# Kernel optimization log

Measured on AMD Instinct MI355X. Metric: run time of the kernel, lower is better.

Reference implementation:

```python
import jax, jax.numpy as jnp
import numpy as np

B, D, S = 16384, 2048, 512      # batch, input_dim, sideinfo_dim
E, H1, H2 = 8, 1024, 512        # subexpert_num, subexpert_unit
EPS = 1e-5                       # BatchNorm eps (torch default)


def setup_inputs() -> dict:
    key = jax.random.key(0)
    ks = jax.random.split(key, 16)
    inp = {
        "input": jax.random.normal(ks[0], (B, D), jnp.float32),
        "sideinfo": jax.random.normal(ks[1], (B, S), jnp.float32),
        # expert layer 1: Linear(D->H1) per expert, batched over E
        "W1": jax.random.normal(ks[2], (E, D, H1), jnp.float32) / np.sqrt(D),
        "b1": jax.random.normal(ks[3], (E, H1), jnp.float32) * 0.01,
        "gamma1": 1.0 + 0.01 * jax.random.normal(ks[4], (E, H1), jnp.float32),
        "beta1": jax.random.normal(ks[5], (E, H1), jnp.float32) * 0.01,
        "mean1": jax.random.normal(ks[6], (E, H1), jnp.float32) * 0.01,
        "var1": jax.random.uniform(ks[7], (E, H1), jnp.float32, 0.5, 1.5),
        # expert layer 2: Linear(H1->H2) per expert
        "W2": jax.random.normal(ks[8], (E, H1, H2), jnp.float32) / np.sqrt(H1),
        "b2": jax.random.normal(ks[9], (E, H2), jnp.float32) * 0.01,
        "gamma2": 1.0 + 0.01 * jax.random.normal(ks[10], (E, H2), jnp.float32),
        "beta2": jax.random.normal(ks[11], (E, H2), jnp.float32) * 0.01,
        "mean2": jax.random.normal(ks[12], (E, H2), jnp.float32) * 0.01,
        "var2": jax.random.uniform(ks[13], (E, H2), jnp.float32, 0.5, 1.5),
        # gate: Linear(S->E) + softmax
        "Wg": jax.random.normal(ks[14], (S, E), jnp.float32) / np.sqrt(S),
        "bg": jax.random.normal(ks[15], (E,), jnp.float32) * 0.01,
    }
    return inp


def _bn(x, gamma, beta, mean, var):
    # eval-mode BatchNorm1d with per-expert running stats; x: [B,E,H]
    return (x - mean) * (gamma * jax.lax.rsqrt(var + EPS)) + beta


def reference(input, sideinfo, W1, b1, gamma1, beta1, mean1, var1,
              W2, b2, gamma2, beta2, mean2, var2, Wg, bg):
    # all E expert MLPs as two batched GEMMs (dropout is identity in eval)
    h = jnp.einsum('bd,edh->beh', input, W1) + b1            # [B,E,H1]
    h = jax.nn.relu(_bn(h, gamma1, beta1, mean1, var1))
    o = jnp.einsum('beh,eho->beo', h, W2) + b2               # [B,E,H2]
    o = jax.nn.relu(_bn(o, gamma2, beta2, mean2, var2))
    gate = jax.nn.softmax(sideinfo @ Wg + bg, axis=1)        # [B,E]
    return jnp.einsum('beo,be->bo', o, gate)                 # [B,H2]
```

## Files before the change

### kernel.cpp

```cpp
#include <hip/hip_runtime.h>
#include <hip/hip_bf16.h>

static constexpr int B_  = 16384;
static constexpr int D_  = 2048;
static constexpr int S_  = 512;
static constexpr int E_  = 8;
static constexpr int H1_ = 1024;
static constexpr int H2_ = 512;
static constexpr float EPS_ = 1e-5f;

typedef __bf16 bf16x8 __attribute__((ext_vector_type(8)));
typedef float  f32x4  __attribute__((ext_vector_type(4)));

static __device__ __forceinline__ unsigned short f2bf(float f) {
    unsigned u = __float_as_uint(f);
    unsigned r = (u + 0x7fffu + ((u >> 16) & 1u)) >> 16;
    return (unsigned short)r;
}


__global__ void cvt_bf16_kernel(const float* __restrict__ in, ushort* __restrict__ out, long n) {
    long i = ((long)blockIdx.x * blockDim.x + threadIdx.x) * 4;
    long stride = (long)gridDim.x * blockDim.x * 4;
    for (; i < n; i += stride) {
        float4 v = *(const float4*)(in + i);
        ushort4 o;
        o.x = f2bf(v.x); o.y = f2bf(v.y); o.z = f2bf(v.z); o.w = f2bf(v.w);
        *(ushort4*)(out + i) = o;
    }
}

__global__ void transpose_cvt_kernel(const float* __restrict__ in, ushort* __restrict__ out,
                                     int R, int C) {
    __shared__ float t[64][65];
    int nbr = R >> 6, nbc = C >> 6;
    int bid = blockIdx.x;
    int e = bid / (nbr * nbc);
    int rem = bid % (nbr * nbc);
    int br = (rem / nbc) << 6, bc = (rem % nbc) << 6;
    const float* ip = in + (size_t)e * R * C;
    ushort* op = out + (size_t)e * R * C;
    int tcol = (threadIdx.x & 15) * 4;
    int trow = threadIdx.x >> 4;
#pragma unroll
    for (int p = 0; p < 4; p++) {
        int r = trow + p * 16;
        float4 v = *(const float4*)(ip + (size_t)(br + r) * C + bc + tcol);
        t[r][tcol + 0] = v.x; t[r][tcol + 1] = v.y; t[r][tcol + 2] = v.z; t[r][tcol + 3] = v.w;
    }
    __syncthreads();
#pragma unroll
    for (int p = 0; p < 4; p++) {
        int c = trow + p * 16;
        ushort4 o;
        o.x = f2bf(t[tcol + 0][c]);
        o.y = f2bf(t[tcol + 1][c]);
        o.z = f2bf(t[tcol + 2][c]);
        o.w = f2bf(t[tcol + 3][c]);
        *(ushort4*)(op + (size_t)(bc + c) * R + br + tcol) = o;
    }
}

__global__ void fold_bn_kernel(const float* __restrict__ gamma, const float* __restrict__ beta,
                               const float* __restrict__ mean, const float* __restrict__ var,
                               const float* __restrict__ bias,
                               float* __restrict__ Sv, float* __restrict__ Tv, int n) {
    int i = blockIdx.x * 256 + threadIdx.x;
    if (i < n) {
        float s = gamma[i] * rsqrtf(var[i] + EPS_);
        Sv[i] = s;
        Tv[i] = (bias[i] - mean[i]) * s + beta[i];
    }
}

__global__ void gate_kernel(const float* __restrict__ side, const float* __restrict__ Wg,
                            const float* __restrict__ bg, float* __restrict__ gate) {
    int wid = threadIdx.x >> 6, lane = threadIdx.x & 63;
    int b = blockIdx.x * 4 + wid;
    const float* sp = side + (size_t)b * S_ + lane * 8;
    float4 v0 = *(const float4*)sp;
    float4 v1 = *(const float4*)(sp + 4);
    float sv[8] = {v0.x, v0.y, v0.z, v0.w, v1.x, v1.y, v1.z, v1.w};
    float acc[E_] = {0,0,0,0,0,0,0,0};
    const float* wrow = Wg + (size_t)(lane * 8) * E_;
#pragma unroll
    for (int j = 0; j < 8; j++) {
        float4 w0 = *(const float4*)(wrow + j * E_);
        float4 w1 = *(const float4*)(wrow + j * E_ + 4);
        acc[0] += sv[j] * w0.x; acc[1] += sv[j] * w0.y;
        acc[2] += sv[j] * w0.z; acc[3] += sv[j] * w0.w;
        acc[4] += sv[j] * w1.x; acc[5] += sv[j] * w1.y;
        acc[6] += sv[j] * w1.z; acc[7] += sv[j] * w1.w;
    }
#pragma unroll
    for (int off = 32; off; off >>= 1)
#pragma unroll
        for (int e = 0; e < E_; e++) acc[e] += __shfl_xor(acc[e], off, 64);
    float m = -1e30f;
#pragma unroll
    for (int e = 0; e < E_; e++) { acc[e] += bg[e]; m = fmaxf(m, acc[e]); }
    float s = 0.f;
#pragma unroll
    for (int e = 0; e < E_; e++) { acc[e] = __expf(acc[e] - m); s += acc[e]; }
    float inv = 1.f / s;
    if (lane < E_) gate[(size_t)b * E_ + lane] = acc[lane] * inv;
}


__device__ __forceinline__ void g2lds16(const void* g, void* l) {
    __builtin_amdgcn_global_load_lds((const __attribute__((address_space(1))) unsigned int*)g,
                                     (__attribute__((address_space(3))) unsigned int*)l,
                                     16, 0, 0);
}

#define BAR()      asm volatile("s_barrier" ::: "memory")
#define WAITVM(n)  asm volatile("s_waitcnt vmcnt(" #n ")" ::: "memory")
#define MFMA(a,b,c) __builtin_amdgcn_mfma_f32_16x16x32_bf16((a),(b),(c),0,0,0)


template<int EPI>
__global__ __launch_bounds__(1024, 4)
void gemm8(const ushort* __restrict__ A, const ushort* __restrict__ Bt, long aBatch,
           const float* __restrict__ Sv, const float* __restrict__ Tv,
           ushort* __restrict__ hout, float* __restrict__ outp, const float* __restrict__ gate,
           int M, int N, int K, int tilesN, int tilesM)
{
    extern __shared__ char smem[];

    const int NT  = K >> 6;
    const int tpe = tilesM * tilesN;

    const int nwg = gridDim.x, per = nwg >> 3;
    const int b0  = blockIdx.x;
    const int bid = (b0 & 7) * per + (b0 >> 3);

    const int e   = bid / tpe;
    const int rem = bid % tpe;
    const int tm  = rem / tilesN, tn = rem % tilesN;

    const char* aBase = (const char*)(A + (size_t)e * aBatch + (size_t)tm * 256 * K);
    const char* bBase = (const char*)(Bt + (size_t)e * N * K + (size_t)tn * 256 * K);
    const size_t rowB = (size_t)K * 2;
    const size_t half1 = 128 * rowB;

    const int tid = threadIdx.x, w = tid >> 6, lane = tid & 63;
    const int wm = w >> 2, wn = w & 3;

    const int srow = tid >> 3;
    const int scol_sw = ((tid & 7) * 16) ^ ((srow & 7) << 4);
    const int ldsW = w * 1024;

    const int lr = lane & 15;
    const int cks0 = ((lane >> 4) * 16) ^ ((lane & 7) << 4);
    const int cks1 = (64 + (lane >> 4) * 16) ^ ((lane & 7) << 4);
    const char* rdA0 = smem + 98304 + (wm * 64 + lr) * 128 + cks0;
    const char* rdA1 = smem + 98304 + (wm * 64 + lr) * 128 + cks1;
    const char* rdB0 = smem + (wn * 64 + lr) * 128 + cks0;
    const char* rdB1 = smem + (wn * 64 + lr) * 128 + cks1;

#define STG2T(gp, ldsoff) do { \
        g2lds16((gp), smem + (ldsoff) + ldsW); \
        g2lds16((gp) + half1, smem + (ldsoff) + 16384 + ldsW); } while (0)

    const char* ga = aBase + (size_t)srow * rowB + scol_sw;
    const char* gb = bBase + (size_t)srow * rowB + scol_sw;

    f32x4 acc[4][4] = {};
    bf16x8 a[4], b[4];

    int bCur = 0, bN1 = 32768, bN2 = 65536;

    STG2T(ga,       98304);
    STG2T(gb,       0);
    STG2T(gb + 128, 32768);
    WAITVM(2);
    BAR();

    const char* spA = ga + 128;
    const char* spB = gb + 256;

    for (int t = 0; t < NT; ++t) {
        const int bi    = t & 1;
        const int oRA   = bi * 32768;
        const int oSA   = 98304 + (bi ^ 1) * 32768;
        const bool moreA = (t < NT - 1);
        const bool moreB = (t < NT - 2);

#pragma unroll
        for (int mf = 0; mf < 4; ++mf) a[mf] = *(const bf16x8*)(rdA0 + oRA + mf * 2048);
#pragma unroll
        for (int nf = 0; nf < 4; ++nf) b[nf] = *(const bf16x8*)(rdB0 + bCur + nf * 2048);
        if (moreA) STG2T(spA, oSA);
        __builtin_amdgcn_s_setprio(1);
#pragma unroll
        for (int mf = 0; mf < 4; ++mf)
#pragma unroll
            for (int nf = 0; nf < 4; ++nf)
                acc[mf][nf] = MFMA(a[mf], b[nf], acc[mf][nf]);
        __builtin_amdgcn_s_setprio(0);

#pragma unroll
        for (int mf = 0; mf < 4; ++mf) a[mf] = *(const bf16x8*)(rdA1 + oRA + mf * 2048);
#pragma unroll
        for (int nf = 0; nf < 4; ++nf) b[nf] = *(const bf16x8*)(rdB1 + bCur + nf * 2048);
        if (moreB) STG2T(spB, bN2);
        __builtin_amdgcn_s_setprio(1);
#pragma unroll
        for (int mf = 0; mf < 4; ++mf)
#pragma unroll
            for (int nf = 0; nf < 4; ++nf)
                acc[mf][nf] = MFMA(a[mf], b[nf], acc[mf][nf]);
        __builtin_amdgcn_s_setprio(0);

        if (moreA) {
            if (moreB) { WAITVM(2); } else { WAITVM(0); }
            BAR();
        }

        spA += 128; spB += 128;
        const int tb = bCur; bCur = bN1; bN1 = bN2; bN2 = tb;
    }

    const int rbase = tm * 256 + wm * 64 + (lane >> 4) * 4;
    const int cbase = tn * 256 + wn * 64 + lr;
    if (EPI == 1) {
#pragma unroll
        for (int nf = 0; nf < 4; ++nf) {
            const int col = cbase + nf * 16;
            const float s = Sv[e * N + col];
            const float tt = Tv[e * N + col];
#pragma unroll
            for (int mf = 0; mf < 4; ++mf) {
                const int row0 = rbase + mf * 16;
                f32x4 v = acc[mf][nf];
#pragma unroll
                for (int r = 0; r < 4; ++r) {
                    float x = v[r] * s + tt;
                    x = x > 0.f ? x : 0.f;
                    hout[((size_t)e * M + row0 + r) * N + col] = f2bf(x);
                }
            }
        }
    }
#undef STG2T
}


__global__ __launch_bounds__(512, 2)
void gemm2e(const ushort* __restrict__ H, const ushort* __restrict__ W2T,
            const float* __restrict__ Sv, const float* __restrict__ Tv,
            const float* __restrict__ gate, float* __restrict__ outp)
{
    extern __shared__ char smem[];

    const int b0 = blockIdx.x;
    const int bid = (b0 & 7) * 32 + (b0 >> 3);
    const int tm = bid >> 1, tn = bid & 1;

    const size_t rowB  = (size_t)H1_ * 2;
    const size_t strAE = (size_t)B_ * H1_ * 2;
    const size_t strBE = (size_t)H2_ * H1_ * 2;
    const size_t half2 = 64 * rowB;
    const size_t halfB = 128 * rowB;

    const int tid = threadIdx.x, w = tid >> 6, lane = tid & 63;
    const int wm = w >> 2, wn = w & 3;

    const int srow = tid >> 3;
    const int scol_sw = ((tid & 7) * 16) ^ ((srow & 7) << 4);
    const int ldsW = w * 1024;

    const int lr = lane & 15;
    const int cks0 = ((lane >> 4) * 16) ^ ((lane & 7) << 4);
    const int cks1 = (64 + (lane >> 4) * 16) ^ ((lane & 7) << 4);
    const char* rdA0 = smem + (wm * 64 + lr) * 128 + cks0;
    const char* rdA1 = smem + (wm * 64 + lr) * 128 + cks1;
    const char* rdB0 = smem + (wn * 64 + lr) * 128 + cks0;
    const char* rdB1 = smem + (wn * 64 + lr) * 128 + cks1;

    const char* ga = (const char*)H + (size_t)tm * 128 * rowB + (size_t)srow * rowB + scol_sw;
    const char* gb = (const char*)W2T + (size_t)tn * 256 * rowB + (size_t)srow * rowB + scol_sw;

#define STG6(gAp, gBp, aOff, bOff) do { \
        g2lds16((gAp),                 smem + (aOff) + 0     + ldsW); \
        g2lds16((gAp) + half2,         smem + (aOff) + 8192  + ldsW); \
        g2lds16((gBp),                 smem + (bOff) + 0     + ldsW); \
        g2lds16((gBp) + half2,         smem + (bOff) + 8192  + ldsW); \
        g2lds16((gBp) + halfB,         smem + (bOff) + 16384 + ldsW); \
        g2lds16((gBp) + halfB + half2, smem + (bOff) + 24576 + ldsW); } while (0)

    f32x4 acc[4][4] = {};
    f32x4 oacc[4][4] = {};
    bf16x8 a0[4], a1[4], b0v[4], b1v[4];

    int aCur = 98304, aN1 = 114688, aN2 = 131072;
    int bCur = 0,     bN1 = 32768,  bN2 = 65536;

    STG6(ga, gb, aCur, bCur);
    STG6(ga + 128, gb + 128, aN1, bN1);
    WAITVM(6);
    BAR();

#pragma unroll
    for (int mf = 0; mf < 4; ++mf) a0[mf] = *(const bf16x8*)(rdA0 + aCur + mf * 2048);
#pragma unroll
    for (int nf = 0; nf < 4; ++nf) b0v[nf] = *(const bf16x8*)(rdB0 + bCur + nf * 2048);

    const int rbase = tm * 128 + wm * 64 + (lane >> 4) * 4;
    const int cbase = tn * 256 + wn * 64 + lr;

    for (int t = 0; t < 128; ++t) {
        const int t2 = t + 2;
        const bool moreS = (t2 < 128);
        const bool moreT = (t < 127);

        const char* gA2 = ga + (size_t)(t2 >> 4) * strAE + (t2 & 15) * 128;
        const char* gB2 = gb + (size_t)(t2 >> 4) * strBE + (t2 & 15) * 128;

#pragma unroll
        for (int mf = 0; mf < 4; ++mf) a1[mf] = *(const bf16x8*)(rdA1 + aCur + mf * 2048);
#pragma unroll
        for (int nf = 0; nf < 4; ++nf) b1v[nf] = *(const bf16x8*)(rdB1 + bCur + nf * 2048);
        if (moreS) STG6(gA2, gB2, aN2, bN2);
        __builtin_amdgcn_s_setprio(1);
#pragma unroll
        for (int mf = 0; mf < 4; ++mf)
#pragma unroll
            for (int nf = 0; nf < 4; ++nf)
                acc[mf][nf] = MFMA(a0[mf], b0v[nf], acc[mf][nf]);
        __builtin_amdgcn_s_setprio(0);

        __builtin_amdgcn_s_setprio(1);
#pragma unroll
        for (int mf = 0; mf < 4; ++mf)
#pragma unroll
            for (int nf = 0; nf < 4; ++nf)
                acc[mf][nf] = MFMA(a1[mf], b1v[nf], acc[mf][nf]);
        __builtin_amdgcn_s_setprio(0);

        if (moreT) {
            if (moreS) { WAITVM(6); } else { WAITVM(0); }
            BAR();
#pragma unroll
            for (int mf = 0; mf < 4; ++mf) a0[mf] = *(const bf16x8*)(rdA0 + aN1 + mf * 2048);
#pragma unroll
            for (int nf = 0; nf < 4; ++nf) b0v[nf] = *(const bf16x8*)(rdB0 + bN1 + nf * 2048);
        }

        if ((t & 15) == 15) {
            const int e = t >> 4;
            float sc[4], tc[4];
#pragma unroll
            for (int nf = 0; nf < 4; ++nf) {
                sc[nf] = Sv[e * H2_ + cbase + nf * 16];
                tc[nf] = Tv[e * H2_ + cbase + nf * 16];
            }
#pragma unroll
            for (int mf = 0; mf < 4; ++mf) {
#pragma unroll
                for (int r = 0; r < 4; ++r) {
                    const int row = rbase + mf * 16 + r;
                    const float g = gate[(size_t)row * E_ + e];
#pragma unroll
                    for (int nf = 0; nf < 4; ++nf) {
                        float x = acc[mf][nf][r] * sc[nf] + tc[nf];
                        x = x > 0.f ? x : 0.f;
                        oacc[mf][nf][r] += g * x;
                    }
                }
            }
#pragma unroll
            for (int mf = 0; mf < 4; ++mf)
#pragma unroll
                for (int nf = 0; nf < 4; ++nf)
                    acc[mf][nf] = (f32x4){0.f, 0.f, 0.f, 0.f};
        }

        const int ta = aCur; aCur = aN1; aN1 = aN2; aN2 = ta;
        const int tb = bCur; bCur = bN1; bN1 = bN2; bN2 = tb;
    }

#pragma unroll
    for (int mf = 0; mf < 4; ++mf) {
#pragma unroll
        for (int r = 0; r < 4; ++r) {
            const int row = rbase + mf * 16 + r;
#pragma unroll
            for (int nf = 0; nf < 4; ++nf)
                outp[(size_t)row * H2_ + cbase + nf * 16] = oacc[mf][nf][r];
        }
    }
#undef STG6
}


extern "C" void kernel_launch(void* const* d_in, const int* in_sizes, int n_in,
                              void* d_out, int out_size, void* d_ws, size_t ws_size,
                              hipStream_t stream) {
    (void)in_sizes; (void)n_in; (void)out_size; (void)ws_size;

    const float* input    = (const float*)d_in[0];
    const float* sideinfo = (const float*)d_in[1];
    const float* W1   = (const float*)d_in[2];
    const float* b1   = (const float*)d_in[3];
    const float* g1   = (const float*)d_in[4];
    const float* be1  = (const float*)d_in[5];
    const float* m1   = (const float*)d_in[6];
    const float* v1   = (const float*)d_in[7];
    const float* W2   = (const float*)d_in[8];
    const float* b2   = (const float*)d_in[9];
    const float* g2   = (const float*)d_in[10];
    const float* be2  = (const float*)d_in[11];
    const float* m2   = (const float*)d_in[12];
    const float* v2   = (const float*)d_in[13];
    const float* Wg   = (const float*)d_in[14];
    const float* bg   = (const float*)d_in[15];

    char* w = (char*)d_ws;
    size_t off = 0;
    auto carve = [&](size_t bytes) {
        void* p = w + off;
        off += (bytes + 255) & ~(size_t)255;
        return p;
    };
    ushort* Abf  = (ushort*)carve((size_t)B_ * D_ * 2);
    ushort* W1T  = (ushort*)carve((size_t)E_ * H1_ * D_ * 2);
    ushort* W2T  = (ushort*)carve((size_t)E_ * H2_ * H1_ * 2);
    ushort* hbuf = (ushort*)carve((size_t)E_ * B_ * H1_ * 2);
    float*  S1   = (float*)carve((size_t)E_ * H1_ * 4);
    float*  T1   = (float*)carve((size_t)E_ * H1_ * 4);
    float*  S2   = (float*)carve((size_t)E_ * H2_ * 4);
    float*  T2   = (float*)carve((size_t)E_ * H2_ * 4);
    float*  gatep = (float*)carve((size_t)B_ * E_ * 4);

    float* outp = (float*)d_out;

    hipFuncSetAttribute(reinterpret_cast<const void*>(&gemm8<1>),
                        hipFuncAttributeMaxDynamicSharedMemorySize, 163840);
    hipFuncSetAttribute(reinterpret_cast<const void*>(&gemm2e),
                        hipFuncAttributeMaxDynamicSharedMemorySize, 147456);

    cvt_bf16_kernel<<<4096, 256, 0, stream>>>(input, Abf, (long)B_ * D_);
    transpose_cvt_kernel<<<E_ * (D_ / 64) * (H1_ / 64), 256, 0, stream>>>(W1, W1T, D_, H1_);
    transpose_cvt_kernel<<<E_ * (H1_ / 64) * (H2_ / 64), 256, 0, stream>>>(W2, W2T, H1_, H2_);
    fold_bn_kernel<<<(E_ * H1_ + 255) / 256, 256, 0, stream>>>(g1, be1, m1, v1, b1, S1, T1, E_ * H1_);
    fold_bn_kernel<<<(E_ * H2_ + 255) / 256, 256, 0, stream>>>(g2, be2, m2, v2, b2, S2, T2, E_ * H2_);
    gate_kernel<<<B_ / 4, 256, 0, stream>>>(sideinfo, Wg, bg, gatep);

    gemm8<1><<<E_ * (B_ / 256) * (H1_ / 256), 1024, 163840, stream>>>(
        Abf, W1T, 0L, S1, T1, hbuf, nullptr, nullptr, B_, H1_, D_, H1_ / 256, B_ / 256);

    gemm2e<<<(B_ / 128) * (H2_ / 256), 512, 147456, stream>>>(
        hbuf, W2T, S2, T2, gatep, outp);
}
```

Baseline: 695.9 us.

## Double gemm2e waves to 16 with 32-row warp tiles and fewer registers

The second expert GEMM now runs with 1024 threads (16 waves) per block instead of 512. Each wave covers a 32x64 output tile instead of 64x64, and the staging macro issues three 16-byte global-to-LDS loads per thread instead of six. The register prefetch of the next k-step's fragments across the barrier is removed; both k-halves are now read from LDS inside the iteration. This halves per-wave accumulator and fragment registers to raise wave count and latency hiding, at the cost of losing the cross-barrier LDS prefetch and adding LDS read traffic per MFMA.

```diff
diff --git a/kernel.cpp b/kernel.cpp
--- a/kernel.cpp
+++ b/kernel.cpp
@@ -246,7 +246,7 @@
 }
 
 
-__global__ __launch_bounds__(512, 2)
+__global__ __launch_bounds__(1024, 4)
 void gemm2e(const ushort* __restrict__ H, const ushort* __restrict__ W2T,
             const float* __restrict__ Sv, const float* __restrict__ Tv,
             const float* __restrict__ gate, float* __restrict__ outp)
@@ -260,7 +260,6 @@
     const size_t rowB  = (size_t)H1_ * 2;
     const size_t strAE = (size_t)B_ * H1_ * 2;
     const size_t strBE = (size_t)H2_ * H1_ * 2;
-    const size_t half2 = 64 * rowB;
     const size_t halfB = 128 * rowB;
 
     const int tid = threadIdx.x, w = tid >> 6, lane = tid & 63;
@@ -273,40 +272,32 @@
     const int lr = lane & 15;
     const int cks0 = ((lane >> 4) * 16) ^ ((lane & 7) << 4);
     const int cks1 = (64 + (lane >> 4) * 16) ^ ((lane & 7) << 4);
-    const char* rdA0 = smem + (wm * 64 + lr) * 128 + cks0;
-    const char* rdA1 = smem + (wm * 64 + lr) * 128 + cks1;
+    const char* rdA0 = smem + 98304 + (wm * 32 + lr) * 128 + cks0;
+    const char* rdA1 = smem + 98304 + (wm * 32 + lr) * 128 + cks1;
     const char* rdB0 = smem + (wn * 64 + lr) * 128 + cks0;
     const char* rdB1 = smem + (wn * 64 + lr) * 128 + cks1;
 
     const char* ga = (const char*)H + (size_t)tm * 128 * rowB + (size_t)srow * rowB + scol_sw;
     const char* gb = (const char*)W2T + (size_t)tn * 256 * rowB + (size_t)srow * rowB + scol_sw;
 
-#define STG6(gAp, gBp, aOff, bOff) do { \
-        g2lds16((gAp),                 smem + (aOff) + 0     + ldsW); \
-        g2lds16((gAp) + half2,         smem + (aOff) + 8192  + ldsW); \
-        g2lds16((gBp),                 smem + (bOff) + 0     + ldsW); \
-        g2lds16((gBp) + half2,         smem + (bOff) + 8192  + ldsW); \
-        g2lds16((gBp) + halfB,         smem + (bOff) + 16384 + ldsW); \
-        g2lds16((gBp) + halfB + half2, smem + (bOff) + 24576 + ldsW); } while (0)
-
-    f32x4 acc[4][4] = {};
-    f32x4 oacc[4][4] = {};
-    bf16x8 a0[4], a1[4], b0v[4], b1v[4];
-
-    int aCur = 98304, aN1 = 114688, aN2 = 131072;
-    int bCur = 0,     bN1 = 32768,  bN2 = 65536;
-
-    STG6(ga, gb, aCur, bCur);
-    STG6(ga + 128, gb + 128, aN1, bN1);
-    WAITVM(6);
+#define STG3(gAp, gBp, aOff, bOff) do { \
+        g2lds16((gAp),         smem + (aOff) + ldsW); \
+        g2lds16((gBp),         smem + (bOff) + ldsW); \
+        g2lds16((gBp) + halfB, smem + (bOff) + 16384 + ldsW); } while (0)
+
+    f32x4 acc[2][4] = {};
+    f32x4 oacc[2][4] = {};
+    bf16x8 a[2], b[4];
+
+    int aCurR = 0,     aN1R = 16384, aN2R = 32768;
+    int bCur  = 0,     bN1  = 32768, bN2  = 65536;
+
+    STG3(ga, gb, 98304 + aCurR, bCur);
+    STG3(ga + 128, gb + 128, 98304 + aN1R, bN1);
+    WAITVM(3);
     BAR();
 
-#pragma unroll
-    for (int mf = 0; mf < 4; ++mf) a0[mf] = *(const bf16x8*)(rdA0 + aCur + mf * 2048);
-#pragma unroll
-    for (int nf = 0; nf < 4; ++nf) b0v[nf] = *(const bf16x8*)(rdB0 + bCur + nf * 2048);
-
-    const int rbase = tm * 128 + wm * 64 + (lane >> 4) * 4;
+    const int rbase = tm * 128 + wm * 32 + (lane >> 4) * 4;
     const int cbase = tn * 256 + wn * 64 + lr;
 
     for (int t = 0; t < 128; ++t) {
@@ -318,33 +309,33 @@
         const char* gB2 = gb + (size_t)(t2 >> 4) * strBE + (t2 & 15) * 128;
 
 #pragma unroll
-        for (int mf = 0; mf < 4; ++mf) a1[mf] = *(const bf16x8*)(rdA1 + aCur + mf * 2048);
-#pragma unroll
-        for (int nf = 0; nf < 4; ++nf) b1v[nf] = *(const bf16x8*)(rdB1 + bCur + nf * 2048);
-        if (moreS) STG6(gA2, gB2, aN2, bN2);
+        for (int mf = 0; mf < 2; ++mf) a[mf] = *(const bf16x8*)(rdA0 + aCurR + mf * 2048);
+#pragma unroll
+        for (int nf = 0; nf < 4; ++nf) b[nf] = *(const bf16x8*)(rdB0 + bCur + nf * 2048);
+        if (moreS) STG3(gA2, gB2, 98304 + aN2R, bN2);
         __builtin_amdgcn_s_setprio(1);
 #pragma unroll
-        for (int mf = 0; mf < 4; ++mf)
+        for (int mf = 0; mf < 2; ++mf)
 #pragma unroll
             for (int nf = 0; nf < 4; ++nf)
-                acc[mf][nf] = MFMA(a0[mf], b0v[nf], acc[mf][nf]);
+                acc[mf][nf] = MFMA(a[mf], b[nf], acc[mf][nf]);
         __builtin_amdgcn_s_setprio(0);
 
+#pragma unroll
+        for (int mf = 0; mf < 2; ++mf) a[mf] = *(const bf16x8*)(rdA1 + aCurR + mf * 2048);
+#pragma unroll
+        for (int nf = 0; nf < 4; ++nf) b[nf] = *(const bf16x8*)(rdB1 + bCur + nf * 2048);
         __builtin_amdgcn_s_setprio(1);
 #pragma unroll
-        for (int mf = 0; mf < 4; ++mf)
+        for (int mf = 0; mf < 2; ++mf)
 #pragma unroll
             for (int nf = 0; nf < 4; ++nf)
-                acc[mf][nf] = MFMA(a1[mf], b1v[nf], acc[mf][nf]);
+                acc[mf][nf] = MFMA(a[mf], b[nf], acc[mf][nf]);
         __builtin_amdgcn_s_setprio(0);
 
         if (moreT) {
-            if (moreS) { WAITVM(6); } else { WAITVM(0); }
+            if (moreS) { WAITVM(3); } else { WAITVM(0); }
             BAR();
-#pragma unroll
-            for (int mf = 0; mf < 4; ++mf) a0[mf] = *(const bf16x8*)(rdA0 + aN1 + mf * 2048);
-#pragma unroll
-            for (int nf = 0; nf < 4; ++nf) b0v[nf] = *(const bf16x8*)(rdB0 + bN1 + nf * 2048);
         }
 
         if ((t & 15) == 15) {
@@ -356,7 +347,7 @@
                 tc[nf] = Tv[e * H2_ + cbase + nf * 16];
             }
 #pragma unroll
-            for (int mf = 0; mf < 4; ++mf) {
+            for (int mf = 0; mf < 2; ++mf) {
 #pragma unroll
                 for (int r = 0; r < 4; ++r) {
                     const int row = rbase + mf * 16 + r;
@@ -370,18 +361,18 @@
                 }
             }
 #pragma unroll
-            for (int mf = 0; mf < 4; ++mf)
+            for (int mf = 0; mf < 2; ++mf)
 #pragma unroll
                 for (int nf = 0; nf < 4; ++nf)
                     acc[mf][nf] = (f32x4){0.f, 0.f, 0.f, 0.f};
         }
 
-        const int ta = aCur; aCur = aN1; aN1 = aN2; aN2 = ta;
-        const int tb = bCur; bCur = bN1; bN1 = bN2; bN2 = tb;
-    }
-
-#pragma unroll
-    for (int mf = 0; mf < 4; ++mf) {
+        const int ta = aCurR; aCurR = aN1R; aN1R = aN2R; aN2R = ta;
+        const int tb = bCur;  bCur  = bN1;  bN1  = bN2;  bN2  = tb;
+    }
+
+#pragma unroll
+    for (int mf = 0; mf < 2; ++mf) {
 #pragma unroll
         for (int r = 0; r < 4; ++r) {
             const int row = rbase + mf * 16 + r;
@@ -390,7 +381,7 @@
                 outp[(size_t)row * H2_ + cbase + nf * 16] = oacc[mf][nf][r];
         }
     }
-#undef STG6
+#undef STG3
 }
 
 
@@ -450,6 +441,6 @@
     gemm8<1><<<E_ * (B_ / 256) * (H1_ / 256), 1024, 163840, stream>>>(
         Abf, W1T, 0L, S1, T1, hbuf, nullptr, nullptr, B_, H1_, D_, H1_ / 256, B_ / 256);
 
-    gemm2e<<<(B_ / 128) * (H2_ / 256), 512, 147456, stream>>>(
+    gemm2e<<<(B_ / 128) * (H2_ / 256), 1024, 147456, stream>>>(
         hbuf, W2T, S2, T2, gatep, outp);
 }
```

Result: no change. 704.6 us (+1.2%).

## Shrink first-layer GEMM tile to 256x128 with K=32 triple-buffered stages

Applied to the files above, without the earlier changes.

Retiles the first expert GEMM from 256x256 output tiles with 1024 threads to 256x128 tiles with 512 threads. The K step drops from 64 to 32, and both A and B now use a three-stage LDS ring. The LDS swizzle is redone for 64-byte rows. Dynamic LDS per block falls from 160KB to 72KB, so two blocks may fit per CU, trading fewer, larger tiles for more, smaller ones. The cost is halved reuse of each A tile, which doubles A reloads from global memory, and twice as many barriers per K.

```diff
diff --git a/kernel.cpp b/kernel.cpp
--- a/kernel.cpp
+++ b/kernel.cpp
@@ -119,7 +119,7 @@
 
 
 template<int EPI>
-__global__ __launch_bounds__(1024, 4)
+__global__ __launch_bounds__(512, 4)
 void gemm8(const ushort* __restrict__ A, const ushort* __restrict__ Bt, long aBatch,
            const float* __restrict__ Sv, const float* __restrict__ Tv,
            ushort* __restrict__ hout, float* __restrict__ outp, const float* __restrict__ gate,
@@ -127,7 +127,7 @@
 {
     extern __shared__ char smem[];
 
-    const int NT  = K >> 6;
+    const int NT  = K >> 5;
     const int tpe = tilesM * tilesN;
 
     const int nwg = gridDim.x, per = nwg >> 3;
@@ -139,28 +139,26 @@
     const int tm  = rem / tilesN, tn = rem % tilesN;
 
     const char* aBase = (const char*)(A + (size_t)e * aBatch + (size_t)tm * 256 * K);
-    const char* bBase = (const char*)(Bt + (size_t)e * N * K + (size_t)tn * 256 * K);
+    const char* bBase = (const char*)(Bt + (size_t)e * N * K + (size_t)tn * 128 * K);
     const size_t rowB = (size_t)K * 2;
-    const size_t half1 = 128 * rowB;
+    const size_t halfA = 128 * rowB;
 
     const int tid = threadIdx.x, w = tid >> 6, lane = tid & 63;
-    const int wm = w >> 2, wn = w & 3;
-
-    const int srow = tid >> 3;
-    const int scol_sw = ((tid & 7) * 16) ^ ((srow & 7) << 4);
+    const int wm = w >> 1, wn = w & 1;
+
+    const int srow = tid >> 2;
+    const int scol_sw = (((tid & 3) ^ ((tid >> 3) & 3)) << 4);
     const int ldsW = w * 1024;
 
     const int lr = lane & 15;
-    const int cks0 = ((lane >> 4) * 16) ^ ((lane & 7) << 4);
-    const int cks1 = (64 + (lane >> 4) * 16) ^ ((lane & 7) << 4);
-    const char* rdA0 = smem + 98304 + (wm * 64 + lr) * 128 + cks0;
-    const char* rdA1 = smem + 98304 + (wm * 64 + lr) * 128 + cks1;
-    const char* rdB0 = smem + (wn * 64 + lr) * 128 + cks0;
-    const char* rdB1 = smem + (wn * 64 + lr) * 128 + cks1;
-
-#define STG2T(gp, ldsoff) do { \
-        g2lds16((gp), smem + (ldsoff) + ldsW); \
-        g2lds16((gp) + half1, smem + (ldsoff) + 16384 + ldsW); } while (0)
+    const int col = ((lane >> 4) * 16) ^ (((lr >> 1) & 3) << 4);
+    const char* rdA = smem + 24576 + (wm * 64 + lr) * 64 + col;
+    const char* rdB = smem + (wn * 64 + lr) * 64 + col;
+
+#define STG3(gAp, gBp, aOff, bOff) do { \
+        g2lds16((gAp),         smem + 24576 + (aOff) + ldsW); \
+        g2lds16((gAp) + halfA, smem + 24576 + (aOff) + 8192 + ldsW); \
+        g2lds16((gBp),         smem + (bOff) + ldsW); } while (0)
 
     const char* ga = aBase + (size_t)srow * rowB + scol_sw;
     const char* gb = bBase + (size_t)srow * rowB + scol_sw;
@@ -168,29 +166,26 @@
     f32x4 acc[4][4] = {};
     bf16x8 a[4], b[4];
 
-    int bCur = 0, bN1 = 32768, bN2 = 65536;
-
-    STG2T(ga,       98304);
-    STG2T(gb,       0);
-    STG2T(gb + 128, 32768);
-    WAITVM(2);
+    int aCur = 0, aN1 = 16384, aN2 = 32768;
+    int bCur = 0, bN1 = 8192,  bN2 = 16384;
+
+    STG3(ga, gb, aCur, bCur);
+    STG3(ga + 64, gb + 64, aN1, bN1);
+    WAITVM(3);
     BAR();
 
     const char* spA = ga + 128;
-    const char* spB = gb + 256;
+    const char* spB = gb + 128;
 
     for (int t = 0; t < NT; ++t) {
-        const int bi    = t & 1;
-        const int oRA   = bi * 32768;
-        const int oSA   = 98304 + (bi ^ 1) * 32768;
-        const bool moreA = (t < NT - 1);
-        const bool moreB = (t < NT - 2);
-
-#pragma unroll
-        for (int mf = 0; mf < 4; ++mf) a[mf] = *(const bf16x8*)(rdA0 + oRA + mf * 2048);
-#pragma unroll
-        for (int nf = 0; nf < 4; ++nf) b[nf] = *(const bf16x8*)(rdB0 + bCur + nf * 2048);
-        if (moreA) STG2T(spA, oSA);
+        const bool moreS = (t < NT - 2);
+        const bool moreT = (t < NT - 1);
+
+#pragma unroll
+        for (int mf = 0; mf < 4; ++mf) a[mf] = *(const bf16x8*)(rdA + aCur + mf * 1024);
+#pragma unroll
+        for (int nf = 0; nf < 4; ++nf) b[nf] = *(const bf16x8*)(rdB + bCur + nf * 1024);
+        if (moreS) STG3(spA, spB, aN2, bN2);
         __builtin_amdgcn_s_setprio(1);
 #pragma unroll
         for (int mf = 0; mf < 4; ++mf)
@@ -199,36 +194,24 @@
                 acc[mf][nf] = MFMA(a[mf], b[nf], acc[mf][nf]);
         __builtin_amdgcn_s_setprio(0);
 
-#pragma unroll
-        for (int mf = 0; mf < 4; ++mf) a[mf] = *(const bf16x8*)(rdA1 + oRA + mf * 2048);
-#pragma unroll
-        for (int nf = 0; nf < 4; ++nf) b[nf] = *(const bf16x8*)(rdB1 + bCur + nf * 2048);
-        if (moreB) STG2T(spB, bN2);
-        __builtin_amdgcn_s_setprio(1);
-#pragma unroll
-        for (int mf = 0; mf < 4; ++mf)
-#pragma unroll
-            for (int nf = 0; nf < 4; ++nf)
-                acc[mf][nf] = MFMA(a[mf], b[nf], acc[mf][nf]);
-        __builtin_amdgcn_s_setprio(0);
-
-        if (moreA) {
-            if (moreB) { WAITVM(2); } else { WAITVM(0); }
+        if (moreT) {
+            if (moreS) { WAITVM(3); } else { WAITVM(0); }
             BAR();
         }
 
-        spA += 128; spB += 128;
+        spA += 64; spB += 64;
+        const int ta = aCur; aCur = aN1; aN1 = aN2; aN2 = ta;
         const int tb = bCur; bCur = bN1; bN1 = bN2; bN2 = tb;
     }
 
     const int rbase = tm * 256 + wm * 64 + (lane >> 4) * 4;
-    const int cbase = tn * 256 + wn * 64 + lr;
+    const int cbase = tn * 128 + wn * 64 + lr;
     if (EPI == 1) {
 #pragma unroll
         for (int nf = 0; nf < 4; ++nf) {
-            const int col = cbase + nf * 16;
-            const float s = Sv[e * N + col];
-            const float tt = Tv[e * N + col];
+            const int colO = cbase + nf * 16;
+            const float s = Sv[e * N + colO];
+            const float tt = Tv[e * N + colO];
 #pragma unroll
             for (int mf = 0; mf < 4; ++mf) {
                 const int row0 = rbase + mf * 16;
@@ -237,12 +220,12 @@
                 for (int r = 0; r < 4; ++r) {
                     float x = v[r] * s + tt;
                     x = x > 0.f ? x : 0.f;
-                    hout[((size_t)e * M + row0 + r) * N + col] = f2bf(x);
+                    hout[((size_t)e * M + row0 + r) * N + colO] = f2bf(x);
                 }
             }
         }
     }
-#undef STG2T
+#undef STG3
 }
 
 
@@ -436,7 +419,7 @@
     float* outp = (float*)d_out;
 
     hipFuncSetAttribute(reinterpret_cast<const void*>(&gemm8<1>),
-                        hipFuncAttributeMaxDynamicSharedMemorySize, 163840);
+                        hipFuncAttributeMaxDynamicSharedMemorySize, 73728);
     hipFuncSetAttribute(reinterpret_cast<const void*>(&gemm2e),
                         hipFuncAttributeMaxDynamicSharedMemorySize, 147456);
 
@@ -447,8 +430,8 @@
     fold_bn_kernel<<<(E_ * H2_ + 255) / 256, 256, 0, stream>>>(g2, be2, m2, v2, b2, S2, T2, E_ * H2_);
     gate_kernel<<<B_ / 4, 256, 0, stream>>>(sideinfo, Wg, bg, gatep);
 
-    gemm8<1><<<E_ * (B_ / 256) * (H1_ / 256), 1024, 163840, stream>>>(
-        Abf, W1T, 0L, S1, T1, hbuf, nullptr, nullptr, B_, H1_, D_, H1_ / 256, B_ / 256);
+    gemm8<1><<<E_ * (B_ / 256) * (H1_ / 128), 512, 73728, stream>>>(
+        Abf, W1T, 0L, S1, T1, hbuf, nullptr, nullptr, B_, H1_, D_, H1_ / 128, B_ / 256);
 
     gemm2e<<<(B_ / 128) * (H2_ / 256), 512, 147456, stream>>>(
         hbuf, W2T, S2, T2, gatep, outp);
```

New measurement: 785.6 us. 1.13x slower.
